# Optimization experiments

Hardware: AMD Instinct MI355X
Metric: run time of the kernel (lower is better)

Reference implementation:

```python
import jax, jax.numpy as jnp
import numpy as np


def _rope_tables(seq_len, head_dim):
    # freqs: [seq_len, head_dim//2]
    inv = 1.0 / (10000.0 ** (jnp.arange(0, head_dim, 2, dtype=jnp.float32) / head_dim))
    pos = jnp.arange(seq_len, dtype=jnp.float32)
    f = jnp.outer(pos, inv)
    return jnp.cos(f), jnp.sin(f)


def _apply_rope(x, cos, sin):
    # x: [B, H, T, D]; interleaved pairs (even, odd) rotated
    x1 = x[..., 0::2]
    x2 = x[..., 1::2]
    r1 = x1 * cos - x2 * sin
    r2 = x1 * sin + x2 * cos
    return jnp.stack([r1, r2], axis=-1).reshape(x.shape)


def setup_inputs() -> dict:
    key = jax.random.key(0)
    k1, k2, k3, k4 = jax.random.split(key, 4)
    B, T, C = 2, 2048, 2048
    s = 1.0 / np.sqrt(C)
    return {
        "x": jax.random.normal(k1, (B, T, C), dtype=jnp.float32),
        "W_qk": jax.random.normal(k2, (C, 2 * C), dtype=jnp.float32) * s,
        "W_v": jax.random.normal(k3, (C, C), dtype=jnp.float32) * s,
        "W_o": jax.random.normal(k4, (C, C), dtype=jnp.float32) * s,
        "n_heads": 16,
    }


def reference(x, W_qk, W_v, W_o, n_heads):
    B, T, C = x.shape
    H = n_heads
    D = C // H
    qk = x @ W_qk                      # [B, T, 2C]
    q, k = jnp.split(qk, 2, axis=-1)
    v = x @ W_v
    q = q.reshape(B, T, H, D).transpose(0, 2, 1, 3)  # [B,H,T,D]
    k = k.reshape(B, T, H, D).transpose(0, 2, 1, 3)
    v = v.reshape(B, T, H, D).transpose(0, 2, 1, 3)
    cos, sin = _rope_tables(T, D)      # [T, D//2]
    q = _apply_rope(q, cos, sin)
    k = _apply_rope(k, cos, sin)
    scores = jnp.einsum("bhqd,bhkd->bhqk", q, k) / jnp.sqrt(jnp.float32(D))
    attn = jax.nn.softmax(scores, axis=-1)
    out = jnp.einsum("bhqk,bhkd->bhqd", attn, v)
    out = out.transpose(0, 2, 1, 3).reshape(B, T, C)
    return out @ W_o, k, v
```

## Files before the change

### kernel.cpp

```cpp
#include <hip/hip_runtime.h>
#include <cstdint>

typedef __bf16 bf16x8 __attribute__((ext_vector_type(8)));
typedef __bf16 bf16x2 __attribute__((ext_vector_type(2)));
typedef float  f32x4  __attribute__((ext_vector_type(4)));
typedef float  f32x16 __attribute__((ext_vector_type(16)));
typedef unsigned int u32;
typedef u32 u32x4 __attribute__((ext_vector_type(4)));
typedef unsigned short u16;

static __device__ __forceinline__ u16 f2bf(float f) {
    u32 u = __float_as_uint(f);
    u += 0x7FFFu + ((u >> 16) & 1u);
    return (u16)(u >> 16);
}

static __device__ __forceinline__ u32 pkbf(float a, float b) {
    bf16x2 v; v[0] = (__bf16)a; v[1] = (__bf16)b;
    return __builtin_bit_cast(u32, v);
}

static __device__ __forceinline__ void glds16(const u16* src, u16* dst) {
    __builtin_amdgcn_global_load_lds((const __attribute__((address_space(1))) void*)src,
                                     (__attribute__((address_space(3))) void*)dst, 16, 0, 0);
}

__global__ void k_cvt(const float* __restrict__ in, u16* __restrict__ out, int n4) {
    int i = blockIdx.x * 256 + threadIdx.x;
    if (i >= n4) return;
    float4 v = ((const float4*)in)[i];
    uint2 o;
    o.x = f2bf(v.x) | ((u32)f2bf(v.y) << 16);
    o.y = f2bf(v.z) | ((u32)f2bf(v.w) << 16);
    ((uint2*)out)[i] = o;
}

__global__ void k_transp(const float* __restrict__ W, u16* __restrict__ Wt, int K, int N) {
    __shared__ float tile[32][33];
    int tx = threadIdx.x & 31, ty = threadIdx.x >> 5;
    int k0 = blockIdx.y * 32, n0 = blockIdx.x * 32;
#pragma unroll
    for (int j = 0; j < 4; ++j)
        tile[ty + j * 8][tx] = W[(size_t)(k0 + ty + j * 8) * N + n0 + tx];
    __syncthreads();
#pragma unroll
    for (int j = 0; j < 4; ++j)
        Wt[(size_t)(n0 + ty + j * 8) * K + k0 + tx] = f2bf(tile[tx][ty + j * 8]);
}

__global__ void k_tables(float* __restrict__ cosT, float* __restrict__ sinT) {
    int i = blockIdx.x * 256 + threadIdx.x;
    int t = i >> 6, d = i & 63;
    double inv = pow(10000.0, -(double)d / 64.0);
    double f = (double)t * inv;
    cosT[i] = (float)cos(f);
    sinT[i] = (float)sin(f);
}

template <int EPI>
__global__ __launch_bounds__(256, 2)
void k_gemm(const u16* __restrict__ A, const u16* __restrict__ Bt,
            float* __restrict__ C, u16* __restrict__ C2,
            int M, int N, int K) {
    __shared__ u16 Al[128 * 32];
    __shared__ u16 Bl[128 * 32];
    const int tid = threadIdx.x;
    const int wv = tid >> 6, ln = tid & 63;
    const int wm = wv >> 1, wn = wv & 1;
    const int lr = ln & 15, lk = ln >> 4;
    const int bm = blockIdx.y, bn = blockIdx.x;
    const u16* Ab = A + (size_t)bm * 128 * K;
    const u16* Bb = Bt + (size_t)bn * 128 * K;
    f32x4 acc[4][4] = {};
    const int c0 = wv * 128 + ln, c1 = c0 + 64;
    const int r0 = c0 >> 2, g0 = c0 & 3, r1 = c1 >> 2, g1 = c1 & 3;
    for (int kt = 0; kt < (K >> 5); ++kt) {
        __syncthreads();
        glds16(Ab + (size_t)r0 * K + kt * 32 + g0 * 8, Al + (wv * 2) * 512);
        glds16(Ab + (size_t)r1 * K + kt * 32 + g1 * 8, Al + (wv * 2 + 1) * 512);
        glds16(Bb + (size_t)r0 * K + kt * 32 + g0 * 8, Bl + (wv * 2) * 512);
        glds16(Bb + (size_t)r1 * K + kt * 32 + g1 * 8, Bl + (wv * 2 + 1) * 512);
        __syncthreads();
        bf16x8 af[4], bfr[4];
#pragma unroll
        for (int m = 0; m < 4; ++m)
            af[m] = *(const bf16x8*)(Al + (wm * 64 + m * 16 + lr) * 32 + lk * 8);
#pragma unroll
        for (int n = 0; n < 4; ++n)
            bfr[n] = *(const bf16x8*)(Bl + (wn * 64 + n * 16 + lr) * 32 + lk * 8);
#pragma unroll
        for (int m = 0; m < 4; ++m)
#pragma unroll
            for (int n = 0; n < 4; ++n)
                acc[m][n] = __builtin_amdgcn_mfma_f32_16x16x32_bf16(af[m], bfr[n], acc[m][n], 0, 0, 0);
    }
    const int gr_base = bm * 128 + wm * 64;
    const int gc_base = bn * 128 + wn * 64;
    if (EPI == 0) {
#pragma unroll
        for (int m = 0; m < 4; ++m) {
            int gr0 = gr_base + m * 16 + lk * 4;
#pragma unroll
            for (int n = 0; n < 4; ++n) {
                int gc = gc_base + n * 16 + lr;
#pragma unroll
                for (int r = 0; r < 4; ++r)
                    C[(size_t)(gr0 + r) * N + gc] = acc[m][n][r];
            }
        }
    } else {
#pragma unroll
        for (int m = 0; m < 4; ++m) {
            int gr0 = gr_base + m * 16 + lk * 4;
            int b_ = gr0 >> 11, t0 = gr0 & 2047;
#pragma unroll
            for (int n = 0; n < 4; ++n) {
                int gc = gc_base + n * 16 + lr;
                int h_ = gc >> 7, d_ = gc & 127;
                float v0 = acc[m][n][0], v1 = acc[m][n][1], v2 = acc[m][n][2], v3 = acc[m][n][3];
                float* vo = C + ((size_t)(b_ * 16 + h_) * 2048 + t0) * 128 + d_;
                vo[0] = v0; vo[128] = v1; vo[256] = v2; vo[384] = v3;
                uint2 pk;
                pk.x = f2bf(v0) | ((u32)f2bf(v1) << 16);
                pk.y = f2bf(v2) | ((u32)f2bf(v3) << 16);
                *(uint2*)(C2 + ((size_t)(b_ * 16 + h_) * 128 + d_) * 2048 + t0) = pk;
            }
        }
    }
}

__global__ void k_rope(const float* __restrict__ qk, const float* __restrict__ cosT,
                       const float* __restrict__ sinT, u16* __restrict__ qb,
                       u16* __restrict__ kb, float* __restrict__ kout) {
    int i = blockIdx.x * 256 + threadIdx.x;
    int p = i & 63;
    int h = (i >> 6) & 15;
    int t = (i >> 10) & 2047;
    int b = i >> 21;
    const float* row = qk + (size_t)((b << 11) + t) * 4096;
    float c = cosT[(t << 6) + p], s = sinT[(t << 6) + p];
    size_t o = ((size_t)((b * 16 + h) * 2048 + t) << 7) + 2 * p;
    float2 q2 = *(const float2*)(row + h * 128 + 2 * p);
    float r1 = q2.x * c - q2.y * s;
    float r2 = q2.x * s + q2.y * c;
    *(u32*)(qb + o) = f2bf(r1) | ((u32)f2bf(r2) << 16);
    float2 k2 = *(const float2*)(row + 2048 + h * 128 + 2 * p);
    r1 = k2.x * c - k2.y * s;
    r2 = k2.x * s + k2.y * c;
    *(u32*)(kb + o) = f2bf(r1) | ((u32)f2bf(r2) << 16);
    *(float2*)(kout + o) = make_float2(r1, r2);
}

__global__ __launch_bounds__(256, 2)
void k_attn(const u16* __restrict__ qb, const u16* __restrict__ kb,
            const u16* __restrict__ vbt, u16* __restrict__ aout) {
    __shared__ u16 Kl[2][64 * 128];
    __shared__ u16 Vl[2][128 * 64];
    __shared__ float scl[4 * 32];
    const int tid = threadIdx.x;
    const int wv = tid >> 6, ln = tid & 63;
    const int lq = ln & 31, hi = ln >> 5;
    const int qt = blockIdx.x, h = blockIdx.y, b = blockIdx.z;
    const size_t bh = (size_t)(b * 16 + h);
    const u16* qbase = qb + bh * 2048 * 128;
    const u16* kbase = kb + bh * 2048 * 128;
    const u16* vbase = vbt + bh * 128 * 2048;
    const int q0 = qt * 128 + wv * 32;
    bf16x8 qf[8];
    {
        const u16* qrow = qbase + (size_t)(q0 + lq) * 128;
#pragma unroll
        for (int t = 0; t < 8; ++t)
            qf[t] = *(const bf16x8*)(qrow + t * 16 + hi * 8);
    }
    f32x16 O[4] = {};
    float m_run = -3.0e38f, l_run = 0.0f;
    const float SCL2 = 0.12751637469644085f;
    const int swz = (lq & 7) << 4;

    auto STAGE = [&](int buf, int kt) {
#pragma unroll
        for (int i = 0; i < 4; ++i) {
            int c = (wv * 4 + i) * 64 + ln;
            int key = c >> 4, g = c & 15;
            glds16(kbase + (size_t)(kt * 64 + key) * 128 + (g ^ (key & 7)) * 8,
                   Kl[buf] + (wv * 4 + i) * 512);
        }
#pragma unroll
        for (int i = 0; i < 4; ++i) {
            int c = (wv * 4 + i) * 64 + ln;
            int dd = c >> 3, g = c & 7;
            glds16(vbase + (size_t)dd * 2048 + kt * 64 + (g ^ (dd & 7)) * 8,
                   Vl[buf] + (wv * 4 + i) * 512);
        }
    };

    STAGE(0, 0);
    __syncthreads();

    for (int kt = 0; kt < 32; ++kt) {
        const int cur = kt & 1;
        if (kt < 31) STAGE(cur ^ 1, kt + 1);
        const char* KlB = (const char*)Kl[cur];
        const char* VlB = (const char*)Vl[cur];
        f32x16 s0 = {}, s1 = {};
#pragma unroll
        for (int t = 0; t < 8; ++t) {
            int off = (t * 32 + hi * 16) ^ swz;
            bf16x8 k0 = *(const bf16x8*)(KlB + lq * 256 + off);
            bf16x8 k1 = *(const bf16x8*)(KlB + (32 + lq) * 256 + off);
            s0 = __builtin_amdgcn_mfma_f32_32x32x16_bf16(k0, qf[t], s0, 0, 0, 0);
            s1 = __builtin_amdgcn_mfma_f32_32x32x16_bf16(k1, qf[t], s1, 0, 0, 0);
        }
        float mt = fmaxf(s0[0], s1[0]);
#pragma unroll
        for (int r = 1; r < 16; ++r) mt = fmaxf(mt, fmaxf(s0[r], s1[r]));
        mt = fmaxf(mt, __shfl_xor(mt, 32));
        if (__any((mt - m_run) * SCL2 > 8.0f)) {
            float m_new = fmaxf(m_run, mt);
            float alpha = exp2f((m_run - m_new) * SCL2);
            if (hi == 0) scl[wv * 32 + lq] = alpha;
            asm volatile("s_waitcnt lgkmcnt(0)" ::: "memory");
#pragma unroll
            for (int t2 = 0; t2 < 4; ++t2) {
                f32x4 a4 = *(const f32x4*)(scl + wv * 32 + t2 * 8 + hi * 4);
#pragma unroll
                for (int n = 0; n < 4; ++n)
#pragma unroll
                    for (int j = 0; j < 4; ++j)
                        O[n][t2 * 4 + j] *= a4[j];
            }
            l_run *= alpha;
            m_run = m_new;
        }
        f32x16 p0, p1;
        float lt = 0.0f;
#pragma unroll
        for (int r = 0; r < 16; ++r) {
            p0[r] = exp2f((s0[r] - m_run) * SCL2);
            p1[r] = exp2f((s1[r] - m_run) * SCL2);
            lt += p0[r] + p1[r];
        }
        lt += __shfl_xor(lt, 32);
        l_run += lt;
        u32 ua[8], ub[8];
#pragma unroll
        for (int a = 0; a < 4; ++a) {
            ua[a]     = pkbf(p0[4 * a + 0], p0[4 * a + 1]);
            ub[a]     = pkbf(p0[4 * a + 2], p0[4 * a + 3]);
            ua[4 + a] = pkbf(p1[4 * a + 0], p1[4 * a + 1]);
            ub[4 + a] = pkbf(p1[4 * a + 2], p1[4 * a + 3]);
        }
#pragma unroll
        for (int t = 0; t < 4; ++t) {
            u32 v0 = hi ? ua[2 * t] : ua[2 * t + 1];
            u32 v1 = hi ? ub[2 * t] : ub[2 * t + 1];
            u32 x0 = (u32)__shfl_xor((int)v0, 32);
            u32 x1 = (u32)__shfl_xor((int)v1, 32);
            u32 o0 = hi ? ua[2 * t + 1] : ua[2 * t];
            u32 o1 = hi ? ub[2 * t + 1] : ub[2 * t];
            u32x4 ww;
            ww.x = hi ? x0 : o0;
            ww.y = hi ? x1 : o1;
            ww.z = hi ? o0 : x0;
            ww.w = hi ? o1 : x1;
            bf16x8 pa = __builtin_bit_cast(bf16x8, ww);
            int koff = (t * 32 + hi * 16);
#pragma unroll
            for (int n = 0; n < 4; ++n) {
                bf16x8 vb = *(const bf16x8*)(VlB + (n * 32 + lq) * 128 + (koff ^ swz));
                O[n] = __builtin_amdgcn_mfma_f32_32x32x16_bf16(pa, vb, O[n], 0, 0, 0);
            }
        }
        __syncthreads();
    }
    float invl = 1.0f / l_run;
    if (hi == 0) scl[wv * 32 + lq] = invl;
    asm volatile("s_waitcnt lgkmcnt(0)" ::: "memory");
#pragma unroll
    for (int t2 = 0; t2 < 4; ++t2) {
        f32x4 iv = *(const f32x4*)(scl + wv * 32 + t2 * 8 + hi * 4);
#pragma unroll
        for (int j = 0; j < 4; ++j) {
            int row = q0 + t2 * 8 + hi * 4 + j;
            u16* orow = aout + (size_t)(b * 2048 + row) * 2048 + h * 128;
#pragma unroll
            for (int n = 0; n < 4; ++n)
                orow[n * 32 + lq] = f2bf(O[n][t2 * 4 + j] * iv[j]);
        }
    }
}

extern "C" void kernel_launch(void* const* d_in, const int* in_sizes, int n_in,
                              void* d_out, int out_size, void* d_ws, size_t ws_size,
                              hipStream_t stream) {
    const float* x   = (const float*)d_in[0];
    const float* Wqk = (const float*)d_in[1];
    const float* Wv  = (const float*)d_in[2];
    const float* Wo  = (const float*)d_in[3];
    float* out0 = (float*)d_out;
    float* kout = out0 + 8388608;
    float* vout = out0 + 16777216;
    char* ws = (char*)d_ws;
    const size_t MB = 1024 * 1024;
    u16*   xb   = (u16*)(ws);
    u16*   wqkT = (u16*)(ws + 16 * MB);
    u16*   wvT  = (u16*)(ws + 32 * MB);
    u16*   woT  = (u16*)(ws + 40 * MB);
    float* cosT = (float*)(ws + 48 * MB);
    float* sinT = (float*)(ws + 48 * MB + 512 * 1024);
    u16*   qbf  = (u16*)(ws + 49 * MB);
    u16*   kbf  = (u16*)(ws + 65 * MB);
    float* qkf  = (float*)(ws + 81 * MB);
    u16*   vbt  = (u16*)(ws + 81 * MB);
    u16*   abf  = (u16*)(ws + 97 * MB);

    k_cvt<<<8192, 256, 0, stream>>>(x, xb, 2097152);
    k_transp<<<dim3(128, 64), 256, 0, stream>>>(Wqk, wqkT, 2048, 4096);
    k_transp<<<dim3(64, 64), 256, 0, stream>>>(Wv, wvT, 2048, 2048);
    k_transp<<<dim3(64, 64), 256, 0, stream>>>(Wo, woT, 2048, 2048);
    k_tables<<<512, 256, 0, stream>>>(cosT, sinT);
    k_gemm<0><<<dim3(32, 32), 256, 0, stream>>>(xb, wqkT, qkf, nullptr, 4096, 4096, 2048);
    k_rope<<<16384, 256, 0, stream>>>(qkf, cosT, sinT, qbf, kbf, kout);
    k_gemm<1><<<dim3(16, 32), 256, 0, stream>>>(xb, wvT, vout, vbt, 4096, 2048, 2048);
    k_attn<<<dim3(16, 16, 2), 256, 0, stream>>>(qbf, kbf, vbt, abf);
    k_gemm<0><<<dim3(16, 32), 256, 0, stream>>>(abf, woT, out0, nullptr, 4096, 2048, 2048);
}
```

Baseline: 475.7 us.

## Replace GEMM with 256x256-tile double-buffered pipelined kernel using swizzled LDS

Replaces the simple 128x128 single-buffered GEMM with a 512-thread, 256x256-tile kernel. It double-buffers 64-wide K slices in 128KB of LDS and overlaps global-to-LDS loads with MFMA work using explicit waitcnt/barrier scheduling and s_setprio. An XOR swizzle is added to reduce LDS bank conflicts. The aim is to hide memory latency and raise operand reuse per tile, at the cost of far fewer blocks (256 or 128 per GEMM), which may underfill 256 CUs, and 128KB of LDS per block, which limits occupancy.

New measurement: 499.0 us. 4.9% more time.

```diff
diff --git a/kernel.cpp b/kernel.cpp
--- a/kernel.cpp
+++ b/kernel.cpp
@@ -58,47 +58,81 @@
 }
 
 template <int EPI>
-__global__ __launch_bounds__(256, 2)
-void k_gemm(const u16* __restrict__ A, const u16* __restrict__ Bt,
-            float* __restrict__ C, u16* __restrict__ C2,
-            int M, int N, int K) {
-    __shared__ u16 Al[128 * 32];
-    __shared__ u16 Bl[128 * 32];
+__global__ __launch_bounds__(512, 2)
+void k_gemm2(const u16* __restrict__ A, const u16* __restrict__ Bt,
+             float* __restrict__ C, u16* __restrict__ C2,
+             int M, int N, int K) {
+    __shared__ u16 lds[65536];
     const int tid = threadIdx.x;
-    const int wv = tid >> 6, ln = tid & 63;
-    const int wm = wv >> 1, wn = wv & 1;
+    const int wid = tid >> 6, ln = tid & 63;
+    const int wm = wid >> 2, wn = wid & 3;
     const int lr = ln & 15, lk = ln >> 4;
     const int bm = blockIdx.y, bn = blockIdx.x;
-    const u16* Ab = A + (size_t)bm * 128 * K;
-    const u16* Bb = Bt + (size_t)bn * 128 * K;
-    f32x4 acc[4][4] = {};
-    const int c0 = wv * 128 + ln, c1 = c0 + 64;
-    const int r0 = c0 >> 2, g0 = c0 & 3, r1 = c1 >> 2, g1 = c1 & 3;
-    for (int kt = 0; kt < (K >> 5); ++kt) {
-        __syncthreads();
-        glds16(Ab + (size_t)r0 * K + kt * 32 + g0 * 8, Al + (wv * 2) * 512);
-        glds16(Ab + (size_t)r1 * K + kt * 32 + g1 * 8, Al + (wv * 2 + 1) * 512);
-        glds16(Bb + (size_t)r0 * K + kt * 32 + g0 * 8, Bl + (wv * 2) * 512);
-        glds16(Bb + (size_t)r1 * K + kt * 32 + g1 * 8, Bl + (wv * 2 + 1) * 512);
-        __syncthreads();
-        bf16x8 af[4], bfr[4];
-#pragma unroll
-        for (int m = 0; m < 4; ++m)
-            af[m] = *(const bf16x8*)(Al + (wm * 64 + m * 16 + lr) * 32 + lk * 8);
-#pragma unroll
-        for (int n = 0; n < 4; ++n)
-            bfr[n] = *(const bf16x8*)(Bl + (wn * 64 + n * 16 + lr) * 32 + lk * 8);
-#pragma unroll
-        for (int m = 0; m < 4; ++m)
-#pragma unroll
-            for (int n = 0; n < 4; ++n)
-                acc[m][n] = __builtin_amdgcn_mfma_f32_16x16x32_bf16(af[m], bfr[n], acc[m][n], 0, 0, 0);
-    }
-    const int gr_base = bm * 128 + wm * 64;
-    const int gc_base = bn * 128 + wn * 64;
+    const u16* Ab = A + (size_t)bm * 256 * K;
+    const u16* Bb = Bt + (size_t)bn * 256 * K;
+    const int nkt = K >> 6;
+    const int r0 = tid >> 2;
+    const int s0 = (tid & 3) ^ ((tid >> 3) & 3);
+    const size_t so0 = (size_t)r0 * K + s0 * 8;
+    const size_t so1 = so0 + (size_t)128 * K;
+    const int dstoff = wid * 512;
+
+#define STA(t, kk) { const u16* s_ = Ab + (size_t)(t) * 64 + (kk) * 32; \
+    u16* d_ = lds + ((t) & 1) * 32768 + (kk) * 8192; \
+    glds16(s_ + so0, d_ + dstoff); glds16(s_ + so1, d_ + 4096 + dstoff); }
+#define STB(t, kk) { const u16* s_ = Bb + (size_t)(t) * 64 + (kk) * 32; \
+    u16* d_ = lds + ((t) & 1) * 32768 + 16384 + (kk) * 8192; \
+    glds16(s_ + so0, d_ + dstoff); glds16(s_ + so1, d_ + 4096 + dstoff); }
+
+    const int lkx8 = (lk ^ ((lr >> 1) & 3)) * 8;
+    const int arow = wm * 128 + lr;
+    const int brow = wn * 64 + lr;
+    f32x4 acc[8][4] = {};
+    bf16x8 af[4], bfr[4];
+
+#define RD(buf, kk, qm) { const u16* ab_ = lds + (buf) * 32768 + (kk) * 8192; \
+    const u16* bb_ = ab_ + 16384; \
+    af[0] = *(const bf16x8*)(ab_ + (arow + ((qm)*4+0)*16) * 32 + lkx8); \
+    af[1] = *(const bf16x8*)(ab_ + (arow + ((qm)*4+1)*16) * 32 + lkx8); \
+    af[2] = *(const bf16x8*)(ab_ + (arow + ((qm)*4+2)*16) * 32 + lkx8); \
+    af[3] = *(const bf16x8*)(ab_ + (arow + ((qm)*4+3)*16) * 32 + lkx8); \
+    bfr[0] = *(const bf16x8*)(bb_ + (brow +  0) * 32 + lkx8); \
+    bfr[1] = *(const bf16x8*)(bb_ + (brow + 16) * 32 + lkx8); \
+    bfr[2] = *(const bf16x8*)(bb_ + (brow + 32) * 32 + lkx8); \
+    bfr[3] = *(const bf16x8*)(bb_ + (brow + 48) * 32 + lkx8); }
+
+#define MM(qm) { __builtin_amdgcn_s_setprio(1); \
+    _Pragma("unroll") for (int mi = 0; mi < 4; ++mi) \
+    _Pragma("unroll") for (int n = 0; n < 4; ++n) \
+        acc[(qm)*4+mi][n] = __builtin_amdgcn_mfma_f32_16x16x32_bf16(af[mi], bfr[n], acc[(qm)*4+mi][n], 0, 0, 0); \
+    __builtin_amdgcn_s_setprio(0); }
+
+#define BAR() __builtin_amdgcn_s_barrier()
+#define LGKM0() asm volatile("s_waitcnt lgkmcnt(0)" ::: "memory")
+#define VMC(nn) asm volatile("s_waitcnt vmcnt(" #nn ")" ::: "memory")
+
+    STA(0, 0); STB(0, 0); STA(0, 1); STB(0, 1); STA(1, 0); STB(1, 0);
+    VMC(4); BAR();
+
+    for (int t = 0; t < nkt; t += 2) {
+        const bool st2 = (t + 2) < nkt, st3 = (t + 3) < nkt;
+        RD(0, 0, 0); STA(t + 1, 1);           BAR(); LGKM0(); MM(0); BAR();
+        RD(0, 0, 1); STB(t + 1, 1);           BAR(); LGKM0(); MM(1); BAR();
+        RD(0, 1, 0); if (st2) STA(t + 2, 0);  BAR(); LGKM0(); MM(0); BAR();
+        RD(0, 1, 1); if (st2) STB(t + 2, 0);  BAR(); LGKM0(); MM(1);
+        if (st2) { VMC(4); } else { VMC(0); } BAR();
+        RD(1, 0, 0); if (st2) STA(t + 2, 1);  BAR(); LGKM0(); MM(0); BAR();
+        RD(1, 0, 1); if (st2) STB(t + 2, 1);  BAR(); LGKM0(); MM(1); BAR();
+        RD(1, 1, 0); if (st3) STA(t + 3, 0);  BAR(); LGKM0(); MM(0); BAR();
+        RD(1, 1, 1); if (st3) STB(t + 3, 0);  BAR(); LGKM0(); MM(1);
+        if (st3) { VMC(4); } BAR();
+    }
+
+    const int gr_base = bm * 256 + wm * 128;
+    const int gc_base = bn * 256 + wn * 64;
     if (EPI == 0) {
 #pragma unroll
-        for (int m = 0; m < 4; ++m) {
+        for (int m = 0; m < 8; ++m) {
             int gr0 = gr_base + m * 16 + lk * 4;
 #pragma unroll
             for (int n = 0; n < 4; ++n) {
@@ -110,7 +144,7 @@
         }
     } else {
 #pragma unroll
-        for (int m = 0; m < 4; ++m) {
+        for (int m = 0; m < 8; ++m) {
             int gr0 = gr_base + m * 16 + lk * 4;
             int b_ = gr0 >> 11, t0 = gr0 & 2047;
 #pragma unroll
@@ -127,6 +161,13 @@
             }
         }
     }
+#undef STA
+#undef STB
+#undef RD
+#undef MM
+#undef BAR
+#undef LGKM0
+#undef VMC
 }
 
 __global__ void k_rope(const float* __restrict__ qk, const float* __restrict__ cosT,
@@ -320,9 +361,9 @@
     k_transp<<<dim3(64, 64), 256, 0, stream>>>(Wv, wvT, 2048, 2048);
     k_transp<<<dim3(64, 64), 256, 0, stream>>>(Wo, woT, 2048, 2048);
     k_tables<<<512, 256, 0, stream>>>(cosT, sinT);
-    k_gemm<0><<<dim3(32, 32), 256, 0, stream>>>(xb, wqkT, qkf, nullptr, 4096, 4096, 2048);
+    k_gemm2<0><<<dim3(16, 16), 512, 0, stream>>>(xb, wqkT, qkf, nullptr, 4096, 4096, 2048);
     k_rope<<<16384, 256, 0, stream>>>(qkf, cosT, sinT, qbf, kbf, kout);
-    k_gemm<1><<<dim3(16, 32), 256, 0, stream>>>(xb, wvT, vout, vbt, 4096, 2048, 2048);
+    k_gemm2<1><<<dim3(8, 16), 512, 0, stream>>>(xb, wvT, vout, vbt, 4096, 2048, 2048);
     k_attn<<<dim3(16, 16, 2), 256, 0, stream>>>(qbf, kbf, vbt, abf);
-    k_gemm<0><<<dim3(16, 32), 256, 0, stream>>>(abf, woT, out0, nullptr, 4096, 2048, 2048);
-}
+    k_gemm2<0><<<dim3(8, 16), 512, 0, stream>>>(abf, woT, out0, nullptr, 4096, 2048, 2048);
+}
```
